# Kernel optimization log

Measured on AMD Instinct MI355X. Metric: run time of the kernel, lower is better.

The kernel has to match this reference:

```python
import jax, jax.numpy as jnp
import numpy as np

N = 100000      # node_size
R = 2000        # rel_size
T = 1000        # time_size
E = 400000      # triple_size (edges)
NNZ = 800000    # nnz of (triple, rel/time) sparse matrices
ADJNNZ = 400000 # nnz of ent/rel/time adjacency matrices
D = 100         # node_hidden (dim)
DEPTH = 2
DOUT = D * (DEPTH + 1)  # 300


def setup_inputs():
    key = jax.random.key(0)
    ks = jax.random.split(key, 24)
    ri = lambda k, n, hi: jax.random.randint(k, (n,), 0, hi, dtype=jnp.int64)
    g = lambda k, shape: jax.random.normal(k, shape, jnp.float32) * 0.05
    adj_input = jnp.stack([ri(ks[0], E, N), ri(ks[1], E, N)], axis=1)
    r_index = jnp.stack([ri(ks[2], NNZ, E), ri(ks[3], NNZ, R)], axis=1)
    t_index = jnp.stack([ri(ks[4], NNZ, E), ri(ks[5], NNZ, T)], axis=1)
    r_val = jax.random.uniform(ks[6], (NNZ,), jnp.float32)
    ent_adj_idx = jnp.stack([ri(ks[7], ADJNNZ, N), ri(ks[8], ADJNNZ, N)], axis=1)
    rel_adj_idx = jnp.stack([ri(ks[9], ADJNNZ, N), ri(ks[10], ADJNNZ, R)], axis=1)
    time_adj_idx = jnp.stack([ri(ks[11], ADJNNZ, N), ri(ks[12], ADJNNZ, T)], axis=1)
    return dict(
        adj_input=adj_input, r_index=r_index, r_val=r_val, t_index=t_index,
        ent_adj_idx=ent_adj_idx, rel_adj_idx=rel_adj_idx, time_adj_idx=time_adj_idx,
        ent_emb=g(ks[13], (N, D)), rel_emb=g(ks[14], (R, D)), time_emb=g(ks[15], (T, D)),
        e_attn=g(ks[16], (DEPTH, D)), e_gate=g(ks[17], (DOUT, DOUT)),
        e_proxy=g(ks[18], (64, DOUT)), e_bias=g(ks[19], (1, DOUT)),
        r_attn=g(ks[20], (DEPTH, D)), r_gate=g(ks[21], (DOUT, DOUT)),
        r_proxy=g(ks[22], (64, DOUT)), r_bias=g(ks[23], (1, DOUT)),
    )


def _l2norm(x):
    # F.normalize(p=2): x / max(||x||, 1e-12)
    return x / jnp.maximum(jnp.linalg.norm(x, axis=-1, keepdims=True), 1e-12)


def _seg_softmax(logits, seg, num):
    # torch.sparse.softmax along rows of the [num, num] sparse matrix
    m = jax.ops.segment_max(logits, seg, num_segments=num)
    e = jnp.exp(logits - m[seg])
    s = jax.ops.segment_sum(e, seg, num_segments=num)
    return e / s[seg]


def _sparse_row_softmax_matmul(idx, emb, nrows):
    # sparse adj with all-ones values + row softmax == row-mean over neighbors
    row, col = idx[:, 0], idx[:, 1]
    cnt = jax.ops.segment_sum(jnp.ones((idx.shape[0],), emb.dtype), row, num_segments=nrows)
    return jax.ops.segment_sum(emb[col] / cnt[row][:, None], row, num_segments=nrows)


def _encoder(features, rel_emb, adj, sp_idx, sp_val, attn, gate_k, proxy, bias):
    feats = jnp.tanh(features)          # activation(features)
    outs = [feats]
    # rels_sum: sparse [E, col] @ rel_emb, then L2-normalize rows (same every layer)
    rels_sum = jax.ops.segment_sum(sp_val[:, None] * rel_emb[sp_idx[:, 1]],
                                   sp_idx[:, 0], num_segments=E)
    rels_sum = _l2norm(rels_sum)        # [E, D]
    row, col = adj[:, 0], adj[:, 1]
    for l in range(DEPTH):
        neighs = feats[col]             # gather [E, D]
        # Householder-like reflection against normalized relation sums
        neighs = neighs - 2.0 * jnp.sum(neighs * rels_sum, axis=1, keepdims=True) * rels_sum
        att = _seg_softmax(rels_sum @ attn[l], row, N)  # sparse softmax over rows
        feats = jnp.tanh(jax.ops.segment_sum(neighs * att[:, None], row, num_segments=N))
        outs.append(feats)
    out = jnp.concatenate(outs, axis=1)  # [N, DOUT]
    pa = jax.nn.softmax(_l2norm(out) @ _l2norm(proxy).T, axis=-1)  # [N, 64]
    pf = out - pa @ proxy
    gate = jax.nn.sigmoid(pf @ gate_k + bias)
    return gate * out + (1.0 - gate) * pf


def reference(adj_input, r_index, r_val, t_index, ent_adj_idx, rel_adj_idx, time_adj_idx,
              ent_emb, rel_emb, time_emb, e_attn, e_gate, e_proxy, e_bias,
              r_attn, r_gate, r_proxy, r_bias):
    ent_f = _sparse_row_softmax_matmul(ent_adj_idx, ent_emb, N)
    rel_f = _sparse_row_softmax_matmul(rel_adj_idx, rel_emb, N)
    time_f = _sparse_row_softmax_matmul(time_adj_idx, time_emb, N)
    out_ent = _encoder(ent_f, rel_emb, adj_input, r_index, r_val, e_attn, e_gate, e_proxy, e_bias)
    out_rel = _encoder(rel_f, rel_emb, adj_input, r_index, r_val, r_attn, r_gate, r_proxy, r_bias)
    out_time = _encoder(time_f, time_emb, adj_input, t_index, r_val, e_attn, e_gate, e_proxy, e_bias)
    # dual_no_time == False path; dropout_rate=0 (eval) => identity
    return jnp.concatenate([out_ent, (out_rel + out_time) / 2.0], axis=-1)
```

## Files before the change

### kernel.cpp

```cpp
#include <hip/hip_runtime.h>
#include <stdint.h>

#define NN    100000
#define EE    400000
#define NNZK  800000
#define ADJK  400000
#define DDIM  100
#define DOUTK 300

typedef unsigned short u16;
typedef unsigned int   u32;
typedef __attribute__((ext_vector_type(8))) short short8;
typedef __attribute__((ext_vector_type(4))) float f32x4;
typedef __attribute__((ext_vector_type(4))) unsigned short u16x4;

__device__ __forceinline__ float bf2f(u16 b) { return __uint_as_float(((u32)b) << 16); }
__device__ __forceinline__ u16 f2bf(float x) {
    u32 u = __float_as_uint(x);
    u32 r = (u + 0x7FFFu + ((u >> 16) & 1u)) >> 16;
    return (u16)r;
}
__device__ __forceinline__ void split_hl(float x, u16& h, u16& l) {
    u32 u = __float_as_uint(x);
    h = (u16)(u >> 16);
    float hf = __uint_as_float(u & 0xFFFF0000u);
    l = (u16)(__float_as_uint(x - hf) >> 16);
}


__global__ __launch_bounds__(256) void k_count(
    const int* __restrict__ idx, int* __restrict__ cnt, int nnz, int kmax)
{
    int i = blockIdx.x * 256 + threadIdx.x;
    if (i >= nnz) return;
    int key = idx[2 * i];
    if (key < 0 || key >= kmax) return;
    atomicAdd(&cnt[key], 1);
}

__global__ __launch_bounds__(256) void k_alloc(
    const int* __restrict__ cnt, int* __restrict__ base, int* __restrict__ cur,
    int* __restrict__ ctr, int n)
{
    int i = blockIdx.x * 256 + threadIdx.x;
    int lane = threadIdx.x & 63;
    int c = (i < n) ? cnt[i] : 0;
    int s = c;
#pragma unroll
    for (int m = 1; m < 64; m <<= 1) {
        int t = __shfl_up(s, m, 64);
        if (lane >= m) s += t;
    }
    int total = __shfl(s, 63, 64);
    int wbase = 0;
    if (lane == 63) wbase = atomicAdd(ctr, total);
    wbase = __shfl(wbase, 63, 64);
    int b = wbase + s - c;
    if (i < n) { base[i] = b; cur[i] = b; }
}

__global__ __launch_bounds__(256) void k_fill(
    const int* __restrict__ idx, const float* __restrict__ val, int* __restrict__ cur,
    int* __restrict__ ocol, float* __restrict__ oval, int* __restrict__ opos,
    int nnz, int kmax)
{
    int i = blockIdx.x * 256 + threadIdx.x;
    if (i >= nnz) return;
    int key = idx[2 * i];
    if (key < 0 || key >= kmax) return;
    int p = atomicAdd(&cur[key], 1);
    ocol[p] = idx[2 * i + 1];
    if (oval) oval[p] = val[i];
    if (opos) opos[i] = p;
}

__global__ __launch_bounds__(256) void rels_build(
    const int* __restrict__ base, const int* __restrict__ cnt,
    const int* __restrict__ rk, const float* __restrict__ rv,
    const int* __restrict__ epos, const int* __restrict__ adjr,
    const float* __restrict__ emb, u16* __restrict__ rels,
    const float* __restrict__ attnA, float* __restrict__ attA0, float* __restrict__ attA1,
    float* __restrict__ denA0, float* __restrict__ denA1,
    const float* __restrict__ attnB, float* __restrict__ attB0, float* __restrict__ attB1,
    float* __restrict__ denB0, float* __restrict__ denB1,
    int kMax, int nE)
{
    int e = blockIdx.x * 8 + (threadIdx.x >> 5);
    if (e >= nE) return;
    int gl = threadIdx.x & 31;
    bool act = gl < 25;
    int d4 = gl * 4;
    int st = base[e], k = cnt[e];
    bool hasB = (attnB != nullptr);

    float4 acc = {0.f, 0.f, 0.f, 0.f};
    for (int j = 0; j < k; ++j) {
        int kk = rk[st + j];
        if (kk < 0 || kk >= kMax) continue;
        float v = rv[st + j];
        if (act) {
            float4 ev = *(const float4*)(emb + (size_t)kk * DDIM + d4);
            acc.x += v * ev.x; acc.y += v * ev.y;
            acc.z += v * ev.z; acc.w += v * ev.w;
        }
    }
    float4 aA0 = {0.f,0.f,0.f,0.f}, aA1 = {0.f,0.f,0.f,0.f};
    float4 aB0 = {0.f,0.f,0.f,0.f}, aB1 = {0.f,0.f,0.f,0.f};
    if (act) {
        aA0 = *(const float4*)(attnA + d4);
        aA1 = *(const float4*)(attnA + DDIM + d4);
        if (hasB) {
            aB0 = *(const float4*)(attnB + d4);
            aB1 = *(const float4*)(attnB + DDIM + d4);
        }
    }
    float s   = acc.x*acc.x + acc.y*acc.y + acc.z*acc.z + acc.w*acc.w;
    float dA0 = acc.x*aA0.x + acc.y*aA0.y + acc.z*aA0.z + acc.w*aA0.w;
    float dA1 = acc.x*aA1.x + acc.y*aA1.y + acc.z*aA1.z + acc.w*aA1.w;
#pragma unroll
    for (int m = 1; m <= 16; m <<= 1) {
        s   += __shfl_xor(s, m, 64);
        dA0 += __shfl_xor(dA0, m, 64);
        dA1 += __shfl_xor(dA1, m, 64);
    }
    float dB0 = 0.f, dB1 = 0.f;
    if (hasB) {
        dB0 = acc.x*aB0.x + acc.y*aB0.y + acc.z*aB0.z + acc.w*aB0.w;
        dB1 = acc.x*aB1.x + acc.y*aB1.y + acc.z*aB1.z + acc.w*aB1.w;
#pragma unroll
        for (int m = 1; m <= 16; m <<= 1) {
            dB0 += __shfl_xor(dB0, m, 64);
            dB1 += __shfl_xor(dB1, m, 64);
        }
    }
    float sc = 1.f / fmaxf(sqrtf(s), 1e-12f);
    int ep = epos[e];
    if (act) {
        u16x4 pk;
        pk[0] = f2bf(acc.x * sc); pk[1] = f2bf(acc.y * sc);
        pk[2] = f2bf(acc.z * sc); pk[3] = f2bf(acc.w * sc);
        *(u16x4*)(rels + (size_t)ep * DDIM + d4) = pk;
    }
    if (gl == 0) {
        int row = adjr[2 * e];
        bool rok = (row >= 0 && row < NN);
        float eA0 = __expf(dA0 * sc), eA1 = __expf(dA1 * sc);
        attA0[ep] = eA0; attA1[ep] = eA1;
        if (rok) { atomicAdd(&denA0[row], eA0); atomicAdd(&denA1[row], eA1); }
        if (hasB) {
            float eB0 = __expf(dB0 * sc), eB1 = __expf(dB1 * sc);
            attB0[ep] = eB0; attB1[ep] = eB1;
            if (rok) { atomicAdd(&denB0[row], eB0); atomicAdd(&denB1[row], eB1); }
        }
    }
}

__global__ __launch_bounds__(256) void feat_gather(
    const int* __restrict__ base, const int* __restrict__ cnt, const int* __restrict__ fcol,
    const float* __restrict__ emb, float* __restrict__ dst, int colMax, int nRows)
{
    int w = blockIdx.x * 8 + (threadIdx.x >> 5);
    if (w >= nRows) return;
    int gl = threadIdx.x & 31;
    bool act = gl < 25;
    int d4 = gl * 4;
    int st = base[w], k = cnt[w];
    float4 acc = {0.f, 0.f, 0.f, 0.f};
    for (int j = 0; j < k; ++j) {
        int col = fcol[st + j];
        if (col < 0 || col >= colMax) continue;
        if (act) {
            float4 ev = *(const float4*)(emb + (size_t)col * DDIM + d4);
            acc.x += ev.x; acc.y += ev.y; acc.z += ev.z; acc.w += ev.w;
        }
    }
    float inv = k ? 1.f / (float)k : 0.f;
    if (act) {
        float4 o;
        o.x = tanhf(acc.x * inv); o.y = tanhf(acc.y * inv);
        o.z = tanhf(acc.z * inv); o.w = tanhf(acc.w * inv);
        *(float4*)(dst + (size_t)w * DOUTK + d4) = o;
    }
}

__global__ __launch_bounds__(256) void mp_layer(
    const int* __restrict__ base, const int* __restrict__ cnt, const int* __restrict__ ecol,
    const u16* __restrict__ rels, const float* __restrict__ att, const float* __restrict__ den,
    const float* __restrict__ src, float* __restrict__ dst, int nRows)
{
    int w = blockIdx.x * 4 + (threadIdx.x >> 6);
    if (w >= nRows) return;
    int lane = threadIdx.x & 63;
    int g = lane >> 5, gl = lane & 31;
    bool act = gl < 25;
    int d4 = gl * 4;
    int st = base[w], k = cnt[w];
    float d = den[w];
    float inv = (d > 0.f) ? 1.f / d : 0.f;
    float4 acc = {0.f, 0.f, 0.f, 0.f};
    for (int j = 0; j < k; j += 2) {
        int je = j + g;
        int col = -1;
        if (je < k) col = ecol[st + je];
        bool cok = (col >= 0 && col < NN);
        float4 r = {0.f,0.f,0.f,0.f}, f = {0.f,0.f,0.f,0.f};
        if (cok && act) {
            u16x4 rr = *(const u16x4*)(rels + (size_t)(st + je) * DDIM + d4);
            r.x = bf2f(rr[0]); r.y = bf2f(rr[1]);
            r.z = bf2f(rr[2]); r.w = bf2f(rr[3]);
            f = *(const float4*)(src + (size_t)col * DOUTK + d4);
        }
        float pd = f.x*r.x + f.y*r.y + f.z*r.z + f.w*r.w;
#pragma unroll
        for (int m = 1; m <= 16; m <<= 1) pd += __shfl_xor(pd, m, 64);
        float a = cok ? att[st + je] * inv : 0.f;
        float c2 = 2.f * pd;
        acc.x += a * (f.x - c2 * r.x);
        acc.y += a * (f.y - c2 * r.y);
        acc.z += a * (f.z - c2 * r.z);
        acc.w += a * (f.w - c2 * r.w);
    }
    acc.x += __shfl_xor(acc.x, 32, 64);
    acc.y += __shfl_xor(acc.y, 32, 64);
    acc.z += __shfl_xor(acc.z, 32, 64);
    acc.w += __shfl_xor(acc.w, 32, 64);
    if (g == 0 && act) {
        float4 o;
        o.x = tanhf(acc.x); o.y = tanhf(acc.y);
        o.z = tanhf(acc.z); o.w = tanhf(acc.w);
        *(float4*)(dst + (size_t)w * DOUTK + d4) = o;
    }
}

__global__ __launch_bounds__(64) void proxy_norms(const float* __restrict__ proxy, float* __restrict__ pn)
{
    int k = threadIdx.x;
    if (k >= 64) return;
    float s = 0.f;
    for (int i = 0; i < DOUTK; ++i) { float v = proxy[k * DOUTK + i]; s += v * v; }
    pn[k] = 1.f / fmaxf(sqrtf(s), 1e-12f);
}

__global__ __launch_bounds__(256) void pack_proxyT(const float* __restrict__ p, u16* __restrict__ o)
{
    int t = blockIdx.x * 256 + threadIdx.x;
    if (t >= 40 * 64 * 8) return;
    int j = t & 7, n = (t >> 3) & 63, kt = t >> 9;
    int k = kt * 8 + j;
    o[t] = f2bf((k < 300) ? p[n * 300 + k] : 0.f);
}
__global__ __launch_bounds__(256) void pack_proxyB(const float* __restrict__ p, u16* __restrict__ o)
{
    int t = blockIdx.x * 256 + threadIdx.x;
    if (t >= 8 * 304 * 8) return;
    int j = t & 7, n = (t >> 3) % 304, kt = t / (304 * 8);
    int k = kt * 8 + j;
    o[t] = f2bf((k < 64 && n < 300) ? p[k * 300 + n] : 0.f);
}
__global__ __launch_bounds__(256) void pack_gateB(const float* __restrict__ p, u16* __restrict__ o)
{
    int t = blockIdx.x * 256 + threadIdx.x;
    if (t >= 40 * 304 * 8) return;
    int j = t & 7, n = (t >> 3) % 304, kt = t / (304 * 8);
    int k = kt * 8 + j;
    o[t] = f2bf((k < 300 && n < 300) ? p[k * 300 + n] : 0.f);
}

__global__ __launch_bounds__(512, 6) void epilogue_mfma(
    const float* __restrict__ outbuf, const u16* __restrict__ PT, const u16* __restrict__ PB,
    const u16* __restrict__ GB, const float* __restrict__ pn, const float* __restrict__ bias,
    float* __restrict__ dout, float alpha, int accumulate)
{
    __shared__ u16 s_h[16][324];
    __shared__ u16 s_l[16][324];
    __shared__ float s_pa[16][68];
    __shared__ float s_rn[16], s_pinv[16];

    const int tid = threadIdx.x;
    const int w = tid >> 6, quad = (tid >> 4) & 3, n15 = tid & 15;
    const size_t rowBase = (size_t)blockIdx.x * 16;

    for (int x = tid; x < 16 * 24; x += 512) {
        int r = x / 24, c = 300 + (x - (x / 24) * 24);
        s_h[r][c] = 0; s_l[r][c] = 0;
    }
    for (int x = tid; x < 16 * 75; x += 512) {
        int r = x / 75, c4 = x - r * 75, c = c4 * 4;
        float4 v = *(const float4*)(outbuf + (rowBase + r) * DOUTK + c);
        u16 h0, l0, h1, l1, h2, l2v, h3, l3;
        split_hl(v.x, h0, l0);
        split_hl(v.y, h1, l1);
        split_hl(v.z, h2, l2v);
        split_hl(v.w, h3, l3);
        u16x4 hv = {h0, h1, h2, h3};
        u16x4 lv = {l0, l1, l2v, l3};
        *(u16x4*)&s_h[r][c] = hv;
        *(u16x4*)&s_l[r][c] = lv;
    }
    __syncthreads();

    f32x4 accp = {0.f, 0.f, 0.f, 0.f};
    if (w < 4) {
        for (int kk = 0; kk < 10; ++kk) {
            short8 ah = *(const short8*)&s_h[n15][kk * 32 + quad * 8];
            short8 al = *(const short8*)&s_l[n15][kk * 32 + quad * 8];
            short8 b = *(const short8*)(PT + (((kk * 4 + quad) * 64) + (w * 16 + n15)) * 8);
            accp = __builtin_amdgcn_mfma_f32_16x16x32_bf16(ah, b, accp, 0, 0, 0);
            accp = __builtin_amdgcn_mfma_f32_16x16x32_bf16(al, b, accp, 0, 0, 0);
        }
    } else {
        int r = (tid >> 4) & 15, l = tid & 15;
        float s = 0.f;
        for (int i = l; i < 300; i += 16) {
            float v = bf2f(s_h[r][i]) + bf2f(s_l[r][i]);
            s += v * v;
        }
#pragma unroll
        for (int m = 8; m; m >>= 1) s += __shfl_xor(s, m, 64);
        if (l == 0) s_rn[r] = 1.f / fmaxf(sqrtf(s), 1e-12f);
    }
    __syncthreads();
    if (w < 4) {
        int col = w * 16 + n15;
        float pnc = pn[col];
#pragma unroll
        for (int g = 0; g < 4; ++g) {
            int row = quad * 4 + g;
            s_pa[row][col] = __expf(accp[g] * s_rn[row] * pnc);
        }
    }
    __syncthreads();
    if (w >= 4) {
        int r = (tid >> 4) & 15, l = tid & 15;
        float s = s_pa[r][l] + s_pa[r][l + 16] + s_pa[r][l + 32] + s_pa[r][l + 48];
#pragma unroll
        for (int m = 8; m; m >>= 1) s += __shfl_xor(s, m, 64);
        if (l == 0) s_pinv[r] = 1.f / s;
    }
    __syncthreads();

    f32x4 accf[3];
#pragma unroll
    for (int t = 0; t < 3; ++t) accf[t] = (f32x4){0.f, 0.f, 0.f, 0.f};
    for (int kk = 0; kk < 2; ++kk) {
        short8 ah, al;
        {
            const float* srcp = &s_pa[n15][kk * 32 + quad * 8];
#pragma unroll
            for (int j = 0; j < 8; ++j) {
                float x = srcp[j];
                u32 h = __float_as_uint(x) >> 16;
                float hf = __uint_as_float(h << 16);
                ah[j] = (short)h;
                al[j] = (short)(__float_as_uint(x - hf) >> 16);
            }
        }
#pragma unroll
        for (int t = 0; t < 3; ++t) {
            int nt = w + 8 * t;
            if (nt < 19) {
                short8 b = *(const short8*)(PB + (((kk * 4 + quad) * 304) + (nt * 16 + n15)) * 8);
                accf[t] = __builtin_amdgcn_mfma_f32_16x16x32_bf16(ah, b, accf[t], 0, 0, 0);
                accf[t] = __builtin_amdgcn_mfma_f32_16x16x32_bf16(al, b, accf[t], 0, 0, 0);
            }
        }
    }
#pragma unroll
    for (int t = 0; t < 3; ++t) {
        int nt = w + 8 * t;
        if (nt < 19) {
            int col = nt * 16 + n15;
#pragma unroll
            for (int g = 0; g < 4; ++g) {
                int row = quad * 4 + g;
                float ov = bf2f(s_h[row][col]) + bf2f(s_l[row][col]);
                float v = ov - accf[t][g] * s_pinv[row];
                u16 hh, ll;
                split_hl(v, hh, ll);
                s_h[row][col] = hh;
                s_l[row][col] = ll;
            }
        }
    }
    __syncthreads();

    f32x4 accg[3];
#pragma unroll
    for (int t = 0; t < 3; ++t) accg[t] = (f32x4){0.f, 0.f, 0.f, 0.f};
    for (int kk = 0; kk < 10; ++kk) {
        short8 ah = *(const short8*)&s_h[n15][kk * 32 + quad * 8];
        short8 al = *(const short8*)&s_l[n15][kk * 32 + quad * 8];
#pragma unroll
        for (int t = 0; t < 3; ++t) {
            int nt = w + 8 * t;
            if (nt < 19) {
                short8 b = *(const short8*)(GB + (((kk * 4 + quad) * 304) + (nt * 16 + n15)) * 8);
                accg[t] = __builtin_amdgcn_mfma_f32_16x16x32_bf16(ah, b, accg[t], 0, 0, 0);
                accg[t] = __builtin_amdgcn_mfma_f32_16x16x32_bf16(al, b, accg[t], 0, 0, 0);
            }
        }
    }
#pragma unroll
    for (int t = 0; t < 3; ++t) {
        int nt = w + 8 * t;
        if (nt < 19) {
            int col = nt * 16 + n15;
            if (col < 300) {
                float bb = bias[col];
#pragma unroll
                for (int g = 0; g < 4; ++g) {
                    int row = quad * 4 + g;
                    float z = accg[t][g] + bb;
                    float gg = 1.f / (1.f + __expf(-z));
                    float pv = bf2f(s_h[row][col]) + bf2f(s_l[row][col]);
                    float res = (pv + gg * accf[t][g] * s_pinv[row]) * alpha;
                    float* o = dout + (rowBase + row) * 600 + col;
                    if (accumulate) res += *o;
                    *o = res;
                }
            }
        }
    }
}

extern "C" void kernel_launch(void* const* d_in, const int* in_sizes, int n_in,
                              void* d_out, int out_size, void* d_ws, size_t ws_size,
                              hipStream_t stream)
{
    const int*   adj      = (const int*)d_in[0];
    const int*   r_index  = (const int*)d_in[1];
    const float* r_val    = (const float*)d_in[2];
    const int*   t_index  = (const int*)d_in[3];
    const int*   ent_adj  = (const int*)d_in[4];
    const int*   rel_adj  = (const int*)d_in[5];
    const int*   time_adj = (const int*)d_in[6];
    const float* ent_emb  = (const float*)d_in[7];
    const float* rel_emb  = (const float*)d_in[8];
    const float* time_emb = (const float*)d_in[9];
    const float* e_attn   = (const float*)d_in[10];
    const float* e_gate   = (const float*)d_in[11];
    const float* e_proxy  = (const float*)d_in[12];
    const float* e_bias   = (const float*)d_in[13];
    const float* r_attn   = (const float*)d_in[14];
    const float* r_gate   = (const float*)d_in[15];
    const float* r_proxy  = (const float*)d_in[16];
    const float* r_bias   = (const float*)d_in[17];
    float* out = (float*)d_out;

    char* ws = (char*)d_ws;
    size_t off = 0;
    auto alloc = [&](size_t bytes) { void* p = ws + off; off += (bytes + 255) & ~255ULL; return p; };
    u16* rels     = (u16*)alloc((size_t)EE * DDIM * 2);
    float* outbuf = (float*)alloc((size_t)NN * DOUTK * 4);
    float* attE0  = (float*)alloc((size_t)EE * 4);
    float* attE1  = (float*)alloc((size_t)EE * 4);
    float* attR0  = (float*)alloc((size_t)EE * 4);
    float* attR1  = (float*)alloc((size_t)EE * 4);
    float* denE0  = (float*)alloc((size_t)NN * 4);
    float* denE1  = (float*)alloc((size_t)NN * 4);
    float* denR0  = (float*)alloc((size_t)NN * 4);
    float* denR1  = (float*)alloc((size_t)NN * 4);
    int* adjcnt   = (int*)alloc((size_t)NN * 4);
    int* abase    = (int*)alloc((size_t)NN * 4);
    int* acur     = (int*)alloc((size_t)NN * 4);
    int* ecol     = (int*)alloc((size_t)EE * 4);
    int* epos     = (int*)alloc((size_t)EE * 4);
    int* fcnt     = (int*)alloc((size_t)NN * 4);
    int* fbase    = (int*)alloc((size_t)NN * 4);
    int* fcur     = (int*)alloc((size_t)NN * 4);
    int* fcol     = (int*)alloc((size_t)ADJK * 4);
    int* ctr      = (int*)alloc(256);
    float* pnE    = (float*)alloc(64 * 4);
    float* pnR    = (float*)alloc(64 * 4);
    u16* PT_E     = (u16*)alloc(40 * 64 * 8 * 2);
    u16* PT_R     = (u16*)alloc(40 * 64 * 8 * 2);
    u16* PB_E     = (u16*)alloc(8 * 304 * 8 * 2);
    u16* PB_R     = (u16*)alloc(8 * 304 * 8 * 2);
    u16* GB_E     = (u16*)alloc(40 * 304 * 8 * 2);
    u16* GB_R     = (u16*)alloc(40 * 304 * 8 * 2);

    int*   rcnt  = (int*)outbuf;
    int*   rbase = rcnt + EE;
    int*   rcur  = rbase + EE;
    int*   rk    = rcur + EE;
    float* rv    = (float*)(rk + NNZK);

    proxy_norms<<<1, 64, 0, stream>>>(e_proxy, pnE);
    proxy_norms<<<1, 64, 0, stream>>>(r_proxy, pnR);
    pack_proxyT<<<80, 256, 0, stream>>>(e_proxy, PT_E);
    pack_proxyT<<<80, 256, 0, stream>>>(r_proxy, PT_R);
    pack_proxyB<<<76, 256, 0, stream>>>(e_proxy, PB_E);
    pack_proxyB<<<76, 256, 0, stream>>>(r_proxy, PB_R);
    pack_gateB<<<380, 256, 0, stream>>>(e_gate, GB_E);
    pack_gateB<<<380, 256, 0, stream>>>(r_gate, GB_R);

    hipMemsetAsync(adjcnt, 0, (size_t)NN * 4, stream);
    hipMemsetAsync(ctr, 0, 4, stream);
    k_count<<<(EE + 255) / 256, 256, 0, stream>>>(adj, adjcnt, EE, NN);
    k_alloc<<<(NN + 255) / 256, 256, 0, stream>>>(adjcnt, abase, acur, ctr, NN);
    k_fill<<<(EE + 255) / 256, 256, 0, stream>>>(adj, nullptr, acur, ecol, nullptr, epos, EE, NN);

    auto build_rels = [&](const int* sp, const float* emb, int kMax,
                          const float* attnA, float* aA0, float* aA1, float* dA0, float* dA1,
                          const float* attnB, float* aB0, float* aB1, float* dB0, float* dB1) {
        hipMemsetAsync(rcnt, 0, (size_t)EE * 4, stream);
        hipMemsetAsync(ctr, 0, 4, stream);
        hipMemsetAsync(dA0, 0, (size_t)NN * 4, stream);
        hipMemsetAsync(dA1, 0, (size_t)NN * 4, stream);
        if (attnB) {
            hipMemsetAsync(dB0, 0, (size_t)NN * 4, stream);
            hipMemsetAsync(dB1, 0, (size_t)NN * 4, stream);
        }
        k_count<<<(NNZK + 255) / 256, 256, 0, stream>>>(sp, rcnt, NNZK, EE);
        k_alloc<<<(EE + 255) / 256, 256, 0, stream>>>(rcnt, rbase, rcur, ctr, EE);
        k_fill<<<(NNZK + 255) / 256, 256, 0, stream>>>(sp, r_val, rcur, rk, rv, nullptr, NNZK, EE);
        rels_build<<<(EE + 7) / 8, 256, 0, stream>>>(rbase, rcnt, rk, rv, epos, adj, emb, rels,
                                                     attnA, aA0, aA1, dA0, dA1,
                                                     attnB, aB0, aB1, dB0, dB1, kMax, EE);
    };

    struct Enc {
        const int* fadj; const float* femb; int colMax;
        const float* a0; const float* a1; const float* d0; const float* d1;
        const u16* PT; const u16* PB; const u16* GB; const float* pn; const float* bias;
        int dcol; float alpha; int accum;
    };
    Enc encs[3] = {
        { ent_adj,  ent_emb,  NN,   attE0, attE1, denE0, denE1, PT_E, PB_E, GB_E, pnE, e_bias,   0, 1.0f, 0 },
        { rel_adj,  rel_emb,  2000, attR0, attR1, denR0, denR1, PT_R, PB_R, GB_R, pnR, r_bias, 300, 0.5f, 0 },
        { time_adj, time_emb, 1000, attE0, attE1, denE0, denE1, PT_E, PB_E, GB_E, pnE, e_bias, 300, 0.5f, 1 },
    };

    build_rels(r_index, rel_emb, 2000,
               e_attn, attE0, attE1, denE0, denE1,
               r_attn, attR0, attR1, denR0, denR1);
    for (int c = 0; c < 3; ++c) {
        if (c == 2) {
            build_rels(t_index, time_emb, 1000,
                       e_attn, attE0, attE1, denE0, denE1,
                       nullptr, nullptr, nullptr, nullptr, nullptr);
        }
        const Enc& e = encs[c];

        hipMemsetAsync(fcnt, 0, (size_t)NN * 4, stream);
        hipMemsetAsync(ctr, 0, 4, stream);
        k_count<<<(ADJK + 255) / 256, 256, 0, stream>>>(e.fadj, fcnt, ADJK, NN);
        k_alloc<<<(NN + 255) / 256, 256, 0, stream>>>(fcnt, fbase, fcur, ctr, NN);
        k_fill<<<(ADJK + 255) / 256, 256, 0, stream>>>(e.fadj, nullptr, fcur, fcol, nullptr, nullptr, ADJK, NN);

        feat_gather<<<(NN + 7) / 8, 256, 0, stream>>>(fbase, fcnt, fcol, e.femb, outbuf, e.colMax, NN);
        mp_layer<<<(NN + 3) / 4, 256, 0, stream>>>(abase, adjcnt, ecol, rels, e.a0, e.d0,
                                                   outbuf, outbuf + DDIM, NN);
        mp_layer<<<(NN + 3) / 4, 256, 0, stream>>>(abase, adjcnt, ecol, rels, e.a1, e.d1,
                                                   outbuf + DDIM, outbuf + 2 * DDIM, NN);
        epilogue_mfma<<<NN / 16, 512, 0, stream>>>(outbuf, e.PT, e.PB, e.GB, e.pn, e.bias,
                                                   out + e.dcol, e.alpha, e.accum);
    }
}
```

Baseline: 2.207 ms.

## Fold softmax denominators into attention weights and widen epilogue tile to 32 rows

Adds an att_fold kernel that divides each edge attention weight by its row denominator once, after rels_build. mp_layer therefore no longer reads den or computes a reciprocal per row. The epilogue now processes 32 rows per block with a 2x4 warp grid instead of 16 rows, so all eight warps issue MFMAs in every phase and each B-operand fetch is reused across more rows. This adds a serial per-row loop kernel, raises shared memory per block (about double), and halves the number of blocks, which may lower occupancy.

New measurement: 2.312 ms. 1.05x slower.

```diff
diff --git a/kernel.cpp b/kernel.cpp
--- a/kernel.cpp
+++ b/kernel.cpp
@@ -152,6 +152,32 @@
             attB0[ep] = eB0; attB1[ep] = eB1;
             if (rok) { atomicAdd(&denB0[row], eB0); atomicAdd(&denB1[row], eB1); }
         }
+    }
+}
+
+__global__ __launch_bounds__(256) void att_fold(
+    const int* __restrict__ base, const int* __restrict__ cnt,
+    float* __restrict__ a0, float* __restrict__ a1,
+    const float* __restrict__ d0, const float* __restrict__ d1,
+    float* __restrict__ b0, float* __restrict__ b1,
+    const float* __restrict__ e0, const float* __restrict__ e1, int nRows)
+{
+    int i = blockIdx.x * 256 + threadIdx.x;
+    if (i >= nRows) return;
+    int st = base[i], k = cnt[i];
+    float v0 = d0[i], v1 = d1[i];
+    float i0 = (v0 > 0.f) ? 1.f / v0 : 0.f;
+    float i1 = (v1 > 0.f) ? 1.f / v1 : 0.f;
+    float i2 = 0.f, i3 = 0.f;
+    if (b0) {
+        float w0 = e0[i], w1 = e1[i];
+        i2 = (w0 > 0.f) ? 1.f / w0 : 0.f;
+        i3 = (w1 > 0.f) ? 1.f / w1 : 0.f;
+    }
+    for (int j = 0; j < k; ++j) {
+        a0[st + j] *= i0;
+        a1[st + j] *= i1;
+        if (b0) { b0[st + j] *= i2; b1[st + j] *= i3; }
     }
 }
 
@@ -185,7 +211,7 @@
 
 __global__ __launch_bounds__(256) void mp_layer(
     const int* __restrict__ base, const int* __restrict__ cnt, const int* __restrict__ ecol,
-    const u16* __restrict__ rels, const float* __restrict__ att, const float* __restrict__ den,
+    const u16* __restrict__ rels, const float* __restrict__ att,
     const float* __restrict__ src, float* __restrict__ dst, int nRows)
 {
     int w = blockIdx.x * 4 + (threadIdx.x >> 6);
@@ -195,8 +221,6 @@
     bool act = gl < 25;
     int d4 = gl * 4;
     int st = base[w], k = cnt[w];
-    float d = den[w];
-    float inv = (d > 0.f) ? 1.f / d : 0.f;
     float4 acc = {0.f, 0.f, 0.f, 0.f};
     for (int j = 0; j < k; j += 2) {
         int je = j + g;
@@ -213,7 +237,7 @@
         float pd = f.x*r.x + f.y*r.y + f.z*r.z + f.w*r.w;
 #pragma unroll
         for (int m = 1; m <= 16; m <<= 1) pd += __shfl_xor(pd, m, 64);
-        float a = cok ? att[st + je] * inv : 0.f;
+        float a = cok ? att[st + je] : 0.f;
         float c2 = 2.f * pd;
         acc.x += a * (f.x - c2 * r.x);
         acc.y += a * (f.y - c2 * r.y);
@@ -271,20 +295,21 @@
     const u16* __restrict__ GB, const float* __restrict__ pn, const float* __restrict__ bias,
     float* __restrict__ dout, float alpha, int accumulate)
 {
-    __shared__ u16 s_h[16][324];
-    __shared__ u16 s_l[16][324];
-    __shared__ float s_pa[16][68];
-    __shared__ float s_rn[16], s_pinv[16];
+    __shared__ u16 s_h[32][324];
+    __shared__ u16 s_l[32][324];
+    __shared__ float s_pa[32][68];
+    __shared__ float s_rn[32], s_pinv[32];
 
     const int tid = threadIdx.x;
     const int w = tid >> 6, quad = (tid >> 4) & 3, n15 = tid & 15;
-    const size_t rowBase = (size_t)blockIdx.x * 16;
-
-    for (int x = tid; x < 16 * 24; x += 512) {
+    const int wr = w >> 2, wc = w & 3;
+    const size_t rowBase = (size_t)blockIdx.x * 32;
+
+    for (int x = tid; x < 32 * 24; x += 512) {
         int r = x / 24, c = 300 + (x - (x / 24) * 24);
         s_h[r][c] = 0; s_l[r][c] = 0;
     }
-    for (int x = tid; x < 16 * 75; x += 512) {
+    for (int x = tid; x < 32 * 75; x += 512) {
         int r = x / 75, c4 = x - r * 75, c = c4 * 4;
         float4 v = *(const float4*)(outbuf + (rowBase + r) * DOUTK + c);
         u16 h0, l0, h1, l1, h2, l2v, h3, l3;
@@ -299,17 +324,8 @@
     }
     __syncthreads();
 
-    f32x4 accp = {0.f, 0.f, 0.f, 0.f};
-    if (w < 4) {
-        for (int kk = 0; kk < 10; ++kk) {
-            short8 ah = *(const short8*)&s_h[n15][kk * 32 + quad * 8];
-            short8 al = *(const short8*)&s_l[n15][kk * 32 + quad * 8];
-            short8 b = *(const short8*)(PT + (((kk * 4 + quad) * 64) + (w * 16 + n15)) * 8);
-            accp = __builtin_amdgcn_mfma_f32_16x16x32_bf16(ah, b, accp, 0, 0, 0);
-            accp = __builtin_amdgcn_mfma_f32_16x16x32_bf16(al, b, accp, 0, 0, 0);
-        }
-    } else {
-        int r = (tid >> 4) & 15, l = tid & 15;
+    {
+        int r = tid >> 4, l = tid & 15;
         float s = 0.f;
         for (int i = l; i < 300; i += 16) {
             float v = bf2f(s_h[r][i]) + bf2f(s_l[r][i]);
@@ -320,18 +336,30 @@
         if (l == 0) s_rn[r] = 1.f / fmaxf(sqrtf(s), 1e-12f);
     }
     __syncthreads();
-    if (w < 4) {
-        int col = w * 16 + n15;
+
+    f32x4 accp = {0.f, 0.f, 0.f, 0.f};
+    {
+        const int arow = wr * 16 + n15;
+        for (int kk = 0; kk < 10; ++kk) {
+            short8 ah = *(const short8*)&s_h[arow][kk * 32 + quad * 8];
+            short8 al = *(const short8*)&s_l[arow][kk * 32 + quad * 8];
+            short8 b = *(const short8*)(PT + (((kk * 4 + quad) * 64) + (wc * 16 + n15)) * 8);
+            accp = __builtin_amdgcn_mfma_f32_16x16x32_bf16(ah, b, accp, 0, 0, 0);
+            accp = __builtin_amdgcn_mfma_f32_16x16x32_bf16(al, b, accp, 0, 0, 0);
+        }
+    }
+    {
+        int col = wc * 16 + n15;
         float pnc = pn[col];
 #pragma unroll
         for (int g = 0; g < 4; ++g) {
-            int row = quad * 4 + g;
+            int row = wr * 16 + quad * 4 + g;
             s_pa[row][col] = __expf(accp[g] * s_rn[row] * pnc);
         }
     }
     __syncthreads();
-    if (w >= 4) {
-        int r = (tid >> 4) & 15, l = tid & 15;
+    {
+        int r = tid >> 4, l = tid & 15;
         float s = s_pa[r][l] + s_pa[r][l + 16] + s_pa[r][l + 32] + s_pa[r][l + 48];
 #pragma unroll
         for (int m = 8; m; m >>= 1) s += __shfl_xor(s, m, 64);
@@ -339,13 +367,13 @@
     }
     __syncthreads();
 
-    f32x4 accf[3];
-#pragma unroll
-    for (int t = 0; t < 3; ++t) accf[t] = (f32x4){0.f, 0.f, 0.f, 0.f};
+    f32x4 accf[5];
+#pragma unroll
+    for (int t = 0; t < 5; ++t) accf[t] = (f32x4){0.f, 0.f, 0.f, 0.f};
     for (int kk = 0; kk < 2; ++kk) {
         short8 ah, al;
         {
-            const float* srcp = &s_pa[n15][kk * 32 + quad * 8];
+            const float* srcp = &s_pa[wr * 16 + n15][kk * 32 + quad * 8];
 #pragma unroll
             for (int j = 0; j < 8; ++j) {
                 float x = srcp[j];
@@ -356,8 +384,8 @@
             }
         }
 #pragma unroll
-        for (int t = 0; t < 3; ++t) {
-            int nt = w + 8 * t;
+        for (int t = 0; t < 5; ++t) {
+            int nt = wc + 4 * t;
             if (nt < 19) {
                 short8 b = *(const short8*)(PB + (((kk * 4 + quad) * 304) + (nt * 16 + n15)) * 8);
                 accf[t] = __builtin_amdgcn_mfma_f32_16x16x32_bf16(ah, b, accf[t], 0, 0, 0);
@@ -366,13 +394,13 @@
         }
     }
 #pragma unroll
-    for (int t = 0; t < 3; ++t) {
-        int nt = w + 8 * t;
+    for (int t = 0; t < 5; ++t) {
+        int nt = wc + 4 * t;
         if (nt < 19) {
             int col = nt * 16 + n15;
 #pragma unroll
             for (int g = 0; g < 4; ++g) {
-                int row = quad * 4 + g;
+                int row = wr * 16 + quad * 4 + g;
                 float ov = bf2f(s_h[row][col]) + bf2f(s_l[row][col]);
                 float v = ov - accf[t][g] * s_pinv[row];
                 u16 hh, ll;
@@ -384,32 +412,35 @@
     }
     __syncthreads();
 
-    f32x4 accg[3];
-#pragma unroll
-    for (int t = 0; t < 3; ++t) accg[t] = (f32x4){0.f, 0.f, 0.f, 0.f};
-    for (int kk = 0; kk < 10; ++kk) {
-        short8 ah = *(const short8*)&s_h[n15][kk * 32 + quad * 8];
-        short8 al = *(const short8*)&s_l[n15][kk * 32 + quad * 8];
-#pragma unroll
-        for (int t = 0; t < 3; ++t) {
-            int nt = w + 8 * t;
-            if (nt < 19) {
-                short8 b = *(const short8*)(GB + (((kk * 4 + quad) * 304) + (nt * 16 + n15)) * 8);
-                accg[t] = __builtin_amdgcn_mfma_f32_16x16x32_bf16(ah, b, accg[t], 0, 0, 0);
-                accg[t] = __builtin_amdgcn_mfma_f32_16x16x32_bf16(al, b, accg[t], 0, 0, 0);
+    f32x4 accg[5];
+#pragma unroll
+    for (int t = 0; t < 5; ++t) accg[t] = (f32x4){0.f, 0.f, 0.f, 0.f};
+    {
+        const int arow = wr * 16 + n15;
+        for (int kk = 0; kk < 10; ++kk) {
+            short8 ah = *(const short8*)&s_h[arow][kk * 32 + quad * 8];
+            short8 al = *(const short8*)&s_l[arow][kk * 32 + quad * 8];
+#pragma unroll
+            for (int t = 0; t < 5; ++t) {
+                int nt = wc + 4 * t;
+                if (nt < 19) {
+                    short8 b = *(const short8*)(GB + (((kk * 4 + quad) * 304) + (nt * 16 + n15)) * 8);
+                    accg[t] = __builtin_amdgcn_mfma_f32_16x16x32_bf16(ah, b, accg[t], 0, 0, 0);
+                    accg[t] = __builtin_amdgcn_mfma_f32_16x16x32_bf16(al, b, accg[t], 0, 0, 0);
+                }
             }
         }
     }
 #pragma unroll
-    for (int t = 0; t < 3; ++t) {
-        int nt = w + 8 * t;
+    for (int t = 0; t < 5; ++t) {
+        int nt = wc + 4 * t;
         if (nt < 19) {
             int col = nt * 16 + n15;
             if (col < 300) {
                 float bb = bias[col];
 #pragma unroll
                 for (int g = 0; g < 4; ++g) {
-                    int row = quad * 4 + g;
+                    int row = wr * 16 + quad * 4 + g;
                     float z = accg[t][g] + bb;
                     float gg = 1.f / (1.f + __expf(-z));
                     float pv = bf2f(s_h[row][col]) + bf2f(s_l[row][col]);
@@ -517,18 +548,21 @@
         rels_build<<<(EE + 7) / 8, 256, 0, stream>>>(rbase, rcnt, rk, rv, epos, adj, emb, rels,
                                                      attnA, aA0, aA1, dA0, dA1,
                                                      attnB, aB0, aB1, dB0, dB1, kMax, EE);
+        att_fold<<<(NN + 255) / 256, 256, 0, stream>>>(abase, adjcnt,
+                                                       aA0, aA1, dA0, dA1,
+                                                       aB0, aB1, dB0, dB1, NN);
     };
 
     struct Enc {
         const int* fadj; const float* femb; int colMax;
-        const float* a0; const float* a1; const float* d0; const float* d1;
+        const float* a0; const float* a1;
         const u16* PT; const u16* PB; const u16* GB; const float* pn; const float* bias;
         int dcol; float alpha; int accum;
     };
     Enc encs[3] = {
-        { ent_adj,  ent_emb,  NN,   attE0, attE1, denE0, denE1, PT_E, PB_E, GB_E, pnE, e_bias,   0, 1.0f, 0 },
-        { rel_adj,  rel_emb,  2000, attR0, attR1, denR0, denR1, PT_R, PB_R, GB_R, pnR, r_bias, 300, 0.5f, 0 },
-        { time_adj, time_emb, 1000, attE0, attE1, denE0, denE1, PT_E, PB_E, GB_E, pnE, e_bias, 300, 0.5f, 1 },
+        { ent_adj,  ent_emb,  NN,   attE0, attE1, PT_E, PB_E, GB_E, pnE, e_bias,   0, 1.0f, 0 },
+        { rel_adj,  rel_emb,  2000, attR0, attR1, PT_R, PB_R, GB_R, pnR, r_bias, 300, 0.5f, 0 },
+        { time_adj, time_emb, 1000, attE0, attE1, PT_E, PB_E, GB_E, pnE, e_bias, 300, 0.5f, 1 },
     };
 
     build_rels(r_index, rel_emb, 2000,
@@ -549,11 +583,11 @@
         k_fill<<<(ADJK + 255) / 256, 256, 0, stream>>>(e.fadj, nullptr, fcur, fcol, nullptr, nullptr, ADJK, NN);
 
         feat_gather<<<(NN + 7) / 8, 256, 0, stream>>>(fbase, fcnt, fcol, e.femb, outbuf, e.colMax, NN);
-        mp_layer<<<(NN + 3) / 4, 256, 0, stream>>>(abase, adjcnt, ecol, rels, e.a0, e.d0,
+        mp_layer<<<(NN + 3) / 4, 256, 0, stream>>>(abase, adjcnt, ecol, rels, e.a0,
                                                    outbuf, outbuf + DDIM, NN);
-        mp_layer<<<(NN + 3) / 4, 256, 0, stream>>>(abase, adjcnt, ecol, rels, e.a1, e.d1,
+        mp_layer<<<(NN + 3) / 4, 256, 0, stream>>>(abase, adjcnt, ecol, rels, e.a1,
                                                    outbuf + DDIM, outbuf + 2 * DDIM, NN);
-        epilogue_mfma<<<NN / 16, 512, 0, stream>>>(outbuf, e.PT, e.PB, e.GB, e.pn, e.bias,
+        epilogue_mfma<<<NN / 32, 512, 0, stream>>>(outbuf, e.PT, e.PB, e.GB, e.pn, e.bias,
                                                    out + e.dcol, e.alpha, e.accum);
     }
 }
```
